# Kernel optimization log

Measured on AMD Instinct MI355X. Metric: run time of the kernel, lower is better.

## Reference

```python
import jax, jax.numpy as jnp
import numpy as np

N, D, ED, E, G, S, H = 16384, 128, 32, 262144, 32, 512, 4
HD = D // H

def _ln(x, g, b, eps=1e-5):
    m = jnp.mean(x, -1, keepdims=True)
    v = jnp.mean((x - m) ** 2, -1, keepdims=True)
    return (x - m) * jax.lax.rsqrt(v + eps) * g + b

def setup_inputs() -> dict:
    key = jax.random.key(0)
    ks = jax.random.split(key, 12)
    r = lambda k, sh: jax.random.normal(k, sh, jnp.float32) * 0.02
    return dict(
        x=jax.random.normal(ks[0], (N, D), jnp.float32),
        edge_index=jax.random.randint(ks[1], (2, E), 0, N),
        edge_attr=jax.random.normal(ks[2], (E, ED), jnp.float32),
        batch=jnp.repeat(jnp.arange(G), S),  # equal-size graphs -> dense batch is a reshape
        gnn_g=jnp.ones((D,), jnp.float32), gnn_b=jnp.zeros((D,), jnp.float32),
        msg_w1=r(ks[3], (2 * D + ED, 2 * D)), msg_b1=jnp.zeros((2 * D,), jnp.float32),
        msg_w2=r(ks[4], (2 * D, D)), msg_b2=jnp.zeros((D,), jnp.float32),
        upd_w1=r(ks[5], (2 * D, D)), upd_b1=jnp.zeros((D,), jnp.float32),
        upd_w2=r(ks[6], (D, D)), upd_b2=jnp.zeros((D,), jnp.float32),
        in_w=r(ks[7], (D, 3 * D)), in_b=jnp.zeros((3 * D,), jnp.float32),
        out_w=r(ks[8], (D, D)), out_b=jnp.zeros((D,), jnp.float32),
        ffn_w1=r(ks[9], (D, 2 * D)), ffn_b1=jnp.zeros((2 * D,), jnp.float32),
        ffn_w2=r(ks[10], (2 * D, D)), ffn_b2=jnp.zeros((D,), jnp.float32),
        n1_g=jnp.ones((D,), jnp.float32), n1_b=jnp.zeros((D,), jnp.float32),
        n2_g=jnp.ones((D,), jnp.float32), n2_b=jnp.zeros((D,), jnp.float32),
    )

def reference(x, edge_index, edge_attr, batch, gnn_g, gnn_b,
              msg_w1, msg_b1, msg_w2, msg_b2, upd_w1, upd_b1, upd_w2, upd_b2,
              in_w, in_b, out_w, out_b, ffn_w1, ffn_b1, ffn_w2, ffn_b2,
              n1_g, n1_b, n2_g, n2_b):
    gelu = lambda t: jax.nn.gelu(t, approximate=False)  # torch nn.GELU default (erf)
    src, dst = edge_index[0], edge_index[1]  # PyG: x_j = source, x_i = target
    # --- local GNN (InteractionLayer), dropout=0 ---
    xn = _ln(x, gnn_g, gnn_b)
    msg_in = jnp.concatenate([xn[dst], xn[src], edge_attr], -1)  # [E, 2D+ED]
    msg = gelu(msg_in @ msg_w1 + msg_b1) @ msg_w2 + msg_b2       # [E, D]
    aggr = jax.ops.segment_sum(msg, dst, num_segments=N)          # scatter-add to targets
    h_local = gelu(jnp.concatenate([xn, aggr], -1) @ upd_w1 + upd_b1) @ upd_w2 + upd_b2
    # --- global self-attention over per-graph dense batch (no padding: equal sizes) ---
    hd = x.reshape(G, S, D)
    qkv = hd @ in_w + in_b
    q, k, v = jnp.split(qkv, 3, -1)
    scale = np.float32(1.0 / np.sqrt(HD))
    q = q.reshape(G, S, H, HD) * scale
    k = k.reshape(G, S, H, HD)
    v = v.reshape(G, S, H, HD)
    att = jax.nn.softmax(jnp.einsum('gqhd,gkhd->ghqk', q, k), -1)
    o = jnp.einsum('ghqk,gkhd->gqhd', att, v).reshape(G, S, D)
    h_attn = (o @ out_w + out_b).reshape(N, D)
    # --- residual + norms + FFN ---
    h = _ln(x + h_local + h_attn, n1_g, n1_b)
    h = _ln(h + (gelu(h @ ffn_w1 + ffn_b1) @ ffn_w2 + ffn_b2), n2_g, n2_b)
    return h
```

## Files before the change

### kernel.cpp

```cpp
#include <hip/hip_runtime.h>
#include <cmath>

#define N_NODES 16384
#define DIM 128
#define EDIM 32
#define NEDGE 262144
#define NG 32
#define SEQ 512
#define NH 4
#define HD 32
#define CH 32

#define EB 32
#define K1 288
#define K1P 296
#define H1 256
#define H1P 264
#define HP 136
#define UP 264

typedef __bf16 bf16x8 __attribute__((ext_vector_type(8)));
typedef float f32x4 __attribute__((ext_vector_type(4)));

__device__ __forceinline__ unsigned short f2bf(float f) {
    union { float f; unsigned int u; } v; v.f = f;
    unsigned int r = (v.u + 0x7FFFu + ((v.u >> 16) & 1u)) >> 16;
    return (unsigned short)r;
}
__device__ __forceinline__ float bf2f(unsigned short u) {
    union { unsigned int u; float f; } v; v.u = ((unsigned int)u) << 16;
    return v.f;
}

__device__ __forceinline__ float geluf(float x) {
    float z = 0.7978845608f * (x + 0.044715f * x * x * x);
    float e = __expf(2.0f * z);
    float t = 1.0f - 2.0f / (e + 1.0f);
    return 0.5f * x * (1.0f + t);
}

__device__ __forceinline__ float waveSum(float v) {
#pragma unroll
    for (int m = 1; m < 64; m <<= 1) v += __shfl_xor(v, m, 64);
    return v;
}

__global__ __launch_bounds__(256) void ln_rows_bf2(const float* __restrict__ x,
                                                   const float* __restrict__ g,
                                                   const float* __restrict__ b,
                                                   unsigned short* __restrict__ xn_bf,
                                                   unsigned short* __restrict__ x_bf) {
    int wave = threadIdx.x >> 6;
    int lane = threadIdx.x & 63;
    int row = blockIdx.x * 4 + wave;
    const float* xr = x + (size_t)row * DIM;
    float v0 = xr[lane], v1 = xr[lane + 64];
    unsigned short* xbf = x_bf + (size_t)row * DIM;
    xbf[lane] = f2bf(v0);
    xbf[lane + 64] = f2bf(v1);
    float mean = waveSum(v0 + v1) * (1.0f / 128.0f);
    float d0 = v0 - mean, d1 = v1 - mean;
    float var = waveSum(d0 * d0 + d1 * d1) * (1.0f / 128.0f);
    float r = rsqrtf(var + 1e-5f);
    unsigned short* obf = xn_bf + (size_t)row * DIM;
    obf[lane] = f2bf(d0 * r * g[lane] + b[lane]);
    obf[lane + 64] = f2bf(d1 * r * g[lane + 64] + b[lane + 64]);
}

__global__ __launch_bounds__(256) void conv_attr(const float* __restrict__ a,
                                                 unsigned short* __restrict__ abf) {
    size_t i = ((size_t)blockIdx.x * 256 + threadIdx.x) * 8;
    float4 x0 = *(const float4*)&a[i];
    float4 x1 = *(const float4*)&a[i + 4];
    unsigned short r[8];
    r[0] = f2bf(x0.x); r[1] = f2bf(x0.y); r[2] = f2bf(x0.z); r[3] = f2bf(x0.w);
    r[4] = f2bf(x1.x); r[5] = f2bf(x1.y); r[6] = f2bf(x1.z); r[7] = f2bf(x1.w);
    *(uint4*)&abf[i] = *(const uint4*)r;
}

__global__ __launch_bounds__(256) void conv_weights(
    const float* __restrict__ s0, const float* __restrict__ s1,
    const float* __restrict__ s2, const float* __restrict__ s3,
    const float* __restrict__ s4, const float* __restrict__ s5,
    const float* __restrict__ s6, const float* __restrict__ s7,
    unsigned short* __restrict__ d0, unsigned short* __restrict__ d1,
    unsigned short* __restrict__ d2, unsigned short* __restrict__ d3,
    unsigned short* __restrict__ d4, unsigned short* __restrict__ d5,
    unsigned short* __restrict__ d6, unsigned short* __restrict__ d7) {
    int i = blockIdx.x * 256 + threadIdx.x;
    if (i < 73728)        { int k = i >> 8, n = i & 255;                 d0[n * 288 + k] = f2bf(s0[i]); }
    else if (i < 106496)  { int j = i - 73728;  int k = j >> 7, n = j & 127; d1[n * 256 + k] = f2bf(s1[j]); }
    else if (i < 139264)  { int j = i - 106496; int k = j >> 7, n = j & 127; d2[n * 256 + k] = f2bf(s2[j]); }
    else if (i < 155648)  { int j = i - 139264; int k = j >> 7, n = j & 127; d3[n * 128 + k] = f2bf(s3[j]); }
    else if (i < 204800)  { int j = i - 155648; int k = j / 384, n = j - k * 384; d4[n * 128 + k] = f2bf(s4[j]); }
    else if (i < 221184)  { int j = i - 204800; int k = j >> 7, n = j & 127; d5[n * 128 + k] = f2bf(s5[j]); }
    else if (i < 253952)  { int j = i - 221184; int k = j >> 8, n = j & 255; d6[n * 128 + k] = f2bf(s6[j]); }
    else if (i < 286720)  { int j = i - 253952; int k = j >> 7, n = j & 127; d7[n * 256 + k] = f2bf(s7[j]); }
}

__global__ __launch_bounds__(256, 4) void edge_mlp_mfma(const unsigned short* __restrict__ xn_bf,
                                                        const int* __restrict__ ei,
                                                        const unsigned short* __restrict__ attr_bf,
                                                        const unsigned short* __restrict__ w1t,
                                                        const float* __restrict__ b1,
                                                        const unsigned short* __restrict__ w2t,
                                                        const float* __restrict__ b2,
                                                        float* __restrict__ aggr) {
    __shared__ __align__(16) unsigned short in_s[EB][K1P];
    __shared__ __align__(16) unsigned short h_s[EB][H1P];
    __shared__ int ds[EB], ss[EB];
    int t = threadIdx.x;
    int eb0 = blockIdx.x * EB;
    if (t < EB) ds[t] = ei[NEDGE + eb0 + t];
    else if (t < 2 * EB) ss[t - EB] = ei[eb0 + t - EB];
    __syncthreads();
    for (int idx = t; idx < EB * 36; idx += 256) {
        int e = idx / 36;
        int seg = idx - e * 36;
        const unsigned short* src;
        if (seg < 16)      src = xn_bf + (size_t)ds[e] * DIM + seg * 8;
        else if (seg < 32) src = xn_bf + (size_t)ss[e] * DIM + (seg - 16) * 8;
        else               src = attr_bf + (size_t)(eb0 + e) * EDIM + (seg - 32) * 8;
        *(uint4*)&in_s[e][seg * 8] = *(const uint4*)src;
    }
    __syncthreads();

    int w = t >> 6;
    int lane = t & 63;
    int l15 = lane & 15;
    int kq = lane >> 4;

    f32x4 acc[2][4] = {};
    for (int kk = 0; kk < 9; ++kk) {
        bf16x8 a[2], bw[4];
#pragma unroll
        for (int mi = 0; mi < 2; ++mi)
            a[mi] = *(const bf16x8*)&in_s[mi * 16 + l15][kk * 32 + kq * 8];
#pragma unroll
        for (int ni = 0; ni < 4; ++ni)
            bw[ni] = *(const bf16x8*)&w1t[(size_t)((w << 6) + ni * 16 + l15) * K1 + kk * 32 + kq * 8];
#pragma unroll
        for (int mi = 0; mi < 2; ++mi)
#pragma unroll
            for (int ni = 0; ni < 4; ++ni)
                acc[mi][ni] = __builtin_amdgcn_mfma_f32_16x16x32_bf16(a[mi], bw[ni], acc[mi][ni], 0, 0, 0);
    }
#pragma unroll
    for (int mi = 0; mi < 2; ++mi)
#pragma unroll
        for (int ni = 0; ni < 4; ++ni) {
            int col = (w << 6) + ni * 16 + l15;
            float bias = b1[col];
#pragma unroll
            for (int j = 0; j < 4; ++j) {
                int row = mi * 16 + kq * 4 + j;
                h_s[row][col] = f2bf(geluf(acc[mi][ni][j] + bias));
            }
        }
    __syncthreads();

    f32x4 acc2[2][2] = {};
    for (int kk = 0; kk < 8; ++kk) {
        bf16x8 a2[2], bw2[2];
#pragma unroll
        for (int mi = 0; mi < 2; ++mi)
            a2[mi] = *(const bf16x8*)&h_s[mi * 16 + l15][kk * 32 + kq * 8];
#pragma unroll
        for (int ni = 0; ni < 2; ++ni)
            bw2[ni] = *(const bf16x8*)&w2t[(size_t)((w << 5) + ni * 16 + l15) * H1 + kk * 32 + kq * 8];
#pragma unroll
        for (int mi = 0; mi < 2; ++mi)
#pragma unroll
            for (int ni = 0; ni < 2; ++ni)
                acc2[mi][ni] = __builtin_amdgcn_mfma_f32_16x16x32_bf16(a2[mi], bw2[ni], acc2[mi][ni], 0, 0, 0);
    }
#pragma unroll
    for (int mi = 0; mi < 2; ++mi)
#pragma unroll
        for (int ni = 0; ni < 2; ++ni) {
            int col = (w << 5) + ni * 16 + l15;
            float bias = b2[col];
#pragma unroll
            for (int j = 0; j < 4; ++j) {
                int row = mi * 16 + kq * 4 + j;
                atomicAdd(&aggr[(size_t)ds[row] * DIM + col], acc2[mi][ni][j] + bias);
            }
        }
}

__global__ __launch_bounds__(256, 2) void update_mfma(const unsigned short* __restrict__ xn_bf,
                                                      const float* __restrict__ aggr,
                                                      const unsigned short* __restrict__ uw1t,
                                                      const float* __restrict__ b1,
                                                      const unsigned short* __restrict__ uw2t,
                                                      const float* __restrict__ b2,
                                                      float* __restrict__ h_local) {
    __shared__ __align__(16) unsigned short cat_s[64][UP];
    __shared__ __align__(16) unsigned short hu_s[64][HP];
    int t = threadIdx.x;
    int n0 = blockIdx.x * 64;
    for (int idx = t; idx < 64 * 32; idx += 256) {
        int e = idx >> 5, seg = idx & 31;
        if (seg < 16) {
            *(uint4*)&cat_s[e][seg * 8] = *(const uint4*)&xn_bf[(size_t)(n0 + e) * DIM + seg * 8];
        } else {
            const float* src = &aggr[(size_t)(n0 + e) * DIM + (seg - 16) * 8];
            float4 a0 = *(const float4*)src, a1 = *(const float4*)(src + 4);
            unsigned short r[8] = {f2bf(a0.x), f2bf(a0.y), f2bf(a0.z), f2bf(a0.w),
                                   f2bf(a1.x), f2bf(a1.y), f2bf(a1.z), f2bf(a1.w)};
            *(uint4*)&cat_s[e][128 + (seg - 16) * 8] = *(const uint4*)r;
        }
    }
    __syncthreads();
    int w = t >> 6, lane = t & 63, l15 = lane & 15, kq = lane >> 4;

    f32x4 acc[4][2] = {};
    for (int kk = 0; kk < 8; ++kk) {
        bf16x8 a[4], bw[2];
#pragma unroll
        for (int mi = 0; mi < 4; ++mi)
            a[mi] = *(const bf16x8*)&cat_s[mi * 16 + l15][kk * 32 + kq * 8];
#pragma unroll
        for (int ni = 0; ni < 2; ++ni)
            bw[ni] = *(const bf16x8*)&uw1t[(size_t)((w << 5) + ni * 16 + l15) * 256 + kk * 32 + kq * 8];
#pragma unroll
        for (int mi = 0; mi < 4; ++mi)
#pragma unroll
            for (int ni = 0; ni < 2; ++ni)
                acc[mi][ni] = __builtin_amdgcn_mfma_f32_16x16x32_bf16(a[mi], bw[ni], acc[mi][ni], 0, 0, 0);
    }
#pragma unroll
    for (int mi = 0; mi < 4; ++mi)
#pragma unroll
        for (int ni = 0; ni < 2; ++ni) {
            int col = (w << 5) + ni * 16 + l15;
            float bias = b1[col];
#pragma unroll
            for (int j = 0; j < 4; ++j) {
                int row = mi * 16 + kq * 4 + j;
                hu_s[row][col] = f2bf(geluf(acc[mi][ni][j] + bias));
            }
        }
    __syncthreads();

    f32x4 acc2[4][2] = {};
    for (int kk = 0; kk < 4; ++kk) {
        bf16x8 a2[4], bw2[2];
#pragma unroll
        for (int mi = 0; mi < 4; ++mi)
            a2[mi] = *(const bf16x8*)&hu_s[mi * 16 + l15][kk * 32 + kq * 8];
#pragma unroll
        for (int ni = 0; ni < 2; ++ni)
            bw2[ni] = *(const bf16x8*)&uw2t[(size_t)((w << 5) + ni * 16 + l15) * 128 + kk * 32 + kq * 8];
#pragma unroll
        for (int mi = 0; mi < 4; ++mi)
#pragma unroll
            for (int ni = 0; ni < 2; ++ni)
                acc2[mi][ni] = __builtin_amdgcn_mfma_f32_16x16x32_bf16(a2[mi], bw2[ni], acc2[mi][ni], 0, 0, 0);
    }
#pragma unroll
    for (int mi = 0; mi < 4; ++mi)
#pragma unroll
        for (int ni = 0; ni < 2; ++ni) {
            int col = (w << 5) + ni * 16 + l15;
            float bias = b2[col];
#pragma unroll
            for (int j = 0; j < 4; ++j) {
                int row = mi * 16 + kq * 4 + j;
                h_local[(size_t)(n0 + row) * DIM + col] = acc2[mi][ni][j] + bias;
            }
        }
}

__global__ __launch_bounds__(256, 2) void qkv_mfma(const unsigned short* __restrict__ x_bf,
                                                   const unsigned short* __restrict__ iwt,
                                                   const float* __restrict__ b,
                                                   unsigned short* __restrict__ qkv_bf) {
    __shared__ __align__(16) unsigned short x_s[64][HP];
    int t = threadIdx.x;
    int n0 = blockIdx.x * 64;
    for (int idx = t; idx < 64 * 16; idx += 256) {
        int e = idx >> 4, seg = idx & 15;
        *(uint4*)&x_s[e][seg * 8] = *(const uint4*)&x_bf[(size_t)(n0 + e) * DIM + seg * 8];
    }
    __syncthreads();
    int w = t >> 6, lane = t & 63, l15 = lane & 15, kq = lane >> 4;

    f32x4 acc[4][6] = {};
    for (int kk = 0; kk < 4; ++kk) {
        bf16x8 a[4], bw[6];
#pragma unroll
        for (int mi = 0; mi < 4; ++mi)
            a[mi] = *(const bf16x8*)&x_s[mi * 16 + l15][kk * 32 + kq * 8];
#pragma unroll
        for (int ni = 0; ni < 6; ++ni)
            bw[ni] = *(const bf16x8*)&iwt[(size_t)(w * 96 + ni * 16 + l15) * 128 + kk * 32 + kq * 8];
#pragma unroll
        for (int mi = 0; mi < 4; ++mi)
#pragma unroll
            for (int ni = 0; ni < 6; ++ni)
                acc[mi][ni] = __builtin_amdgcn_mfma_f32_16x16x32_bf16(a[mi], bw[ni], acc[mi][ni], 0, 0, 0);
    }
#pragma unroll
    for (int mi = 0; mi < 4; ++mi)
#pragma unroll
        for (int ni = 0; ni < 6; ++ni) {
            int col = w * 96 + ni * 16 + l15;
            float bias = b[col];
#pragma unroll
            for (int j = 0; j < 4; ++j) {
                int row = mi * 16 + kq * 4 + j;
                qkv_bf[(size_t)(n0 + row) * 384 + col] = f2bf(acc[mi][ni][j] + bias);
            }
        }
}

__global__ __launch_bounds__(256) void attn_flash(const unsigned short* __restrict__ qkv,
                                                  float* __restrict__ o) {
    int bid = blockIdx.x;
    int quarter = bid & 3;
    int h = (bid >> 2) & 3;
    int g = bid >> 4;
    int t = threadIdx.x;
    int qi = t & 127;
    int sp = t >> 7;
    int sq = quarter * 128 + qi;
    int nq = g * SEQ + sq;

    __shared__ __align__(16) float k_s[2][CH][HD];
    __shared__ __align__(16) float v_s[2][CH][HD];
    __shared__ float merge_s[128][34];

    float qv[HD];
    const unsigned short* qr = qkv + (size_t)nq * 384 + h * HD;
#pragma unroll
    for (int d0 = 0; d0 < HD; d0 += 8) {
        uint4 raw = *(const uint4*)&qr[d0];
        const unsigned short* rs = (const unsigned short*)&raw;
#pragma unroll
        for (int j = 0; j < 8; ++j) qv[d0 + j] = bf2f(rs[j]);
    }
    const float scale = 0.17677669529663687f;
#pragma unroll
    for (int d = 0; d < HD; ++d) qv[d] *= scale;

    float m = -1e30f, l = 0.0f;
    float oacc[HD];
#pragma unroll
    for (int d = 0; d < HD; ++d) oacc[d] = 0.0f;

    int base_j = sp * 256;
    int r = qi >> 3;
    int c4 = (qi & 7) * 4;
    for (int c0 = 0; c0 < 256; c0 += CH) {
        __syncthreads();
#pragma unroll
        for (int p = 0; p < CH; p += 16) {
            int j = base_j + c0 + p + r;
            const unsigned short* kr = qkv + (size_t)(g * SEQ + j) * 384 + 128 + h * HD;
            const unsigned short* vr = qkv + (size_t)(g * SEQ + j) * 384 + 256 + h * HD;
            uint2 kraw = *(const uint2*)&kr[c4];
            uint2 vraw = *(const uint2*)&vr[c4];
            const unsigned short* kp = (const unsigned short*)&kraw;
            const unsigned short* vp = (const unsigned short*)&vraw;
            float4 kf = {bf2f(kp[0]), bf2f(kp[1]), bf2f(kp[2]), bf2f(kp[3])};
            float4 vf = {bf2f(vp[0]), bf2f(vp[1]), bf2f(vp[2]), bf2f(vp[3])};
            *(float4*)&k_s[sp][p + r][c4] = kf;
            *(float4*)&v_s[sp][p + r][c4] = vf;
        }
        __syncthreads();
        float sc[CH];
#pragma unroll
        for (int j = 0; j < CH; ++j) {
            float s = 0.0f;
#pragma unroll
            for (int d = 0; d < HD; ++d) s = fmaf(qv[d], k_s[sp][j][d], s);
            sc[j] = s;
        }
        float cm = sc[0];
#pragma unroll
        for (int j = 1; j < CH; ++j) cm = fmaxf(cm, sc[j]);
        float mn = fmaxf(m, cm);
        float corr = __expf(m - mn);
        l *= corr;
#pragma unroll
        for (int d = 0; d < HD; ++d) oacc[d] *= corr;
#pragma unroll
        for (int j = 0; j < CH; ++j) {
            float p = __expf(sc[j] - mn);
            l += p;
#pragma unroll
            for (int d = 0; d < HD; ++d) oacc[d] = fmaf(p, v_s[sp][j][d], oacc[d]);
        }
        m = mn;
    }
    __syncthreads();
    if (sp == 1) {
        merge_s[qi][0] = m;
        merge_s[qi][1] = l;
#pragma unroll
        for (int d = 0; d < HD; ++d) merge_s[qi][2 + d] = oacc[d];
    }
    __syncthreads();
    if (sp == 0) {
        float m1 = merge_s[qi][0], l1 = merge_s[qi][1];
        float mn = fmaxf(m, m1);
        float cc0 = __expf(m - mn), cc1 = __expf(m1 - mn);
        float inv = 1.0f / (cc0 * l + cc1 * l1);
        float* orow = o + (size_t)nq * DIM + h * HD;
#pragma unroll
        for (int d = 0; d < HD; ++d)
            orow[d] = (cc0 * oacc[d] + cc1 * merge_s[qi][2 + d]) * inv;
    }
}

__global__ __launch_bounds__(256, 2) void proj_res_ln_mfma(const float* __restrict__ x,
                                                           const float* __restrict__ h_local,
                                                           const float* __restrict__ o,
                                                           const unsigned short* __restrict__ owt,
                                                           const float* __restrict__ ob,
                                                           const float* __restrict__ g1,
                                                           const float* __restrict__ bb1,
                                                           float* __restrict__ h1) {
    __shared__ __align__(16) unsigned short o_s[64][HP];
    __shared__ float y_s[64][132];
    int t = threadIdx.x;
    int n0 = blockIdx.x * 64;
    for (int idx = t; idx < 64 * 16; idx += 256) {
        int e = idx >> 4, seg = idx & 15;
        const float* src = &o[(size_t)(n0 + e) * DIM + seg * 8];
        float4 a0 = *(const float4*)src, a1 = *(const float4*)(src + 4);
        unsigned short rr[8] = {f2bf(a0.x), f2bf(a0.y), f2bf(a0.z), f2bf(a0.w),
                                f2bf(a1.x), f2bf(a1.y), f2bf(a1.z), f2bf(a1.w)};
        *(uint4*)&o_s[e][seg * 8] = *(const uint4*)rr;
    }
    __syncthreads();
    int w = t >> 6, lane = t & 63, l15 = lane & 15, kq = lane >> 4;

    f32x4 acc[4][2] = {};
    for (int kk = 0; kk < 4; ++kk) {
        bf16x8 a[4], bw[2];
#pragma unroll
        for (int mi = 0; mi < 4; ++mi)
            a[mi] = *(const bf16x8*)&o_s[mi * 16 + l15][kk * 32 + kq * 8];
#pragma unroll
        for (int ni = 0; ni < 2; ++ni)
            bw[ni] = *(const bf16x8*)&owt[(size_t)((w << 5) + ni * 16 + l15) * 128 + kk * 32 + kq * 8];
#pragma unroll
        for (int mi = 0; mi < 4; ++mi)
#pragma unroll
            for (int ni = 0; ni < 2; ++ni)
                acc[mi][ni] = __builtin_amdgcn_mfma_f32_16x16x32_bf16(a[mi], bw[ni], acc[mi][ni], 0, 0, 0);
    }
#pragma unroll
    for (int mi = 0; mi < 4; ++mi)
#pragma unroll
        for (int ni = 0; ni < 2; ++ni) {
            int col = (w << 5) + ni * 16 + l15;
            float bias = ob[col];
#pragma unroll
            for (int j = 0; j < 4; ++j) {
                int row = mi * 16 + kq * 4 + j;
                size_t gi = (size_t)(n0 + row) * DIM + col;
                y_s[row][col] = x[gi] + h_local[gi] + acc[mi][ni][j] + bias;
            }
        }
    __syncthreads();
    for (int rr = 0; rr < 16; ++rr) {
        int row = (w << 4) + rr;
        float v0 = y_s[row][lane], v1 = y_s[row][lane + 64];
        float mean = waveSum(v0 + v1) * (1.0f / 128.0f);
        float d0 = v0 - mean, d1 = v1 - mean;
        float var = waveSum(d0 * d0 + d1 * d1) * (1.0f / 128.0f);
        float rs = rsqrtf(var + 1e-5f);
        float* hrow = h1 + (size_t)(n0 + row) * DIM;
        hrow[lane] = d0 * rs * g1[lane] + bb1[lane];
        hrow[lane + 64] = d1 * rs * g1[lane + 64] + bb1[lane + 64];
    }
}

__global__ __launch_bounds__(256, 1) void ffn_ln_mfma(const float* __restrict__ h1,
                                                      const unsigned short* __restrict__ fw1t,
                                                      const float* __restrict__ fb1,
                                                      const unsigned short* __restrict__ fw2t,
                                                      const float* __restrict__ fb2,
                                                      const float* __restrict__ g2,
                                                      const float* __restrict__ b2n,
                                                      float* __restrict__ out) {
    __shared__ __align__(16) unsigned short h_s[64][HP];
    __shared__ __align__(16) unsigned short hid_s[64][UP];
    __shared__ float y_s[64][132];
    int t = threadIdx.x;
    int n0 = blockIdx.x * 64;
    for (int idx = t; idx < 64 * 16; idx += 256) {
        int e = idx >> 4, seg = idx & 15;
        const float* src = &h1[(size_t)(n0 + e) * DIM + seg * 8];
        float4 a0 = *(const float4*)src, a1 = *(const float4*)(src + 4);
        unsigned short rr[8] = {f2bf(a0.x), f2bf(a0.y), f2bf(a0.z), f2bf(a0.w),
                                f2bf(a1.x), f2bf(a1.y), f2bf(a1.z), f2bf(a1.w)};
        *(uint4*)&h_s[e][seg * 8] = *(const uint4*)rr;
    }
    __syncthreads();
    int w = t >> 6, lane = t & 63, l15 = lane & 15, kq = lane >> 4;

    f32x4 acc[4][4] = {};
    for (int kk = 0; kk < 4; ++kk) {
        bf16x8 a[4], bw[4];
#pragma unroll
        for (int mi = 0; mi < 4; ++mi)
            a[mi] = *(const bf16x8*)&h_s[mi * 16 + l15][kk * 32 + kq * 8];
#pragma unroll
        for (int ni = 0; ni < 4; ++ni)
            bw[ni] = *(const bf16x8*)&fw1t[(size_t)((w << 6) + ni * 16 + l15) * 128 + kk * 32 + kq * 8];
#pragma unroll
        for (int mi = 0; mi < 4; ++mi)
#pragma unroll
            for (int ni = 0; ni < 4; ++ni)
                acc[mi][ni] = __builtin_amdgcn_mfma_f32_16x16x32_bf16(a[mi], bw[ni], acc[mi][ni], 0, 0, 0);
    }
#pragma unroll
    for (int mi = 0; mi < 4; ++mi)
#pragma unroll
        for (int ni = 0; ni < 4; ++ni) {
            int col = (w << 6) + ni * 16 + l15;
            float bias = fb1[col];
#pragma unroll
            for (int j = 0; j < 4; ++j) {
                int row = mi * 16 + kq * 4 + j;
                hid_s[row][col] = f2bf(geluf(acc[mi][ni][j] + bias));
            }
        }
    __syncthreads();

    f32x4 acc2[4][2] = {};
    for (int kk = 0; kk < 8; ++kk) {
        bf16x8 a2[4], bw2[2];
#pragma unroll
        for (int mi = 0; mi < 4; ++mi)
            a2[mi] = *(const bf16x8*)&hid_s[mi * 16 + l15][kk * 32 + kq * 8];
#pragma unroll
        for (int ni = 0; ni < 2; ++ni)
            bw2[ni] = *(const bf16x8*)&fw2t[(size_t)((w << 5) + ni * 16 + l15) * 256 + kk * 32 + kq * 8];
#pragma unroll
        for (int mi = 0; mi < 4; ++mi)
#pragma unroll
            for (int ni = 0; ni < 2; ++ni)
                acc2[mi][ni] = __builtin_amdgcn_mfma_f32_16x16x32_bf16(a2[mi], bw2[ni], acc2[mi][ni], 0, 0, 0);
    }
#pragma unroll
    for (int mi = 0; mi < 4; ++mi)
#pragma unroll
        for (int ni = 0; ni < 2; ++ni) {
            int col = (w << 5) + ni * 16 + l15;
            float bias = fb2[col];
#pragma unroll
            for (int j = 0; j < 4; ++j) {
                int row = mi * 16 + kq * 4 + j;
                y_s[row][col] = h1[(size_t)(n0 + row) * DIM + col] + acc2[mi][ni][j] + bias;
            }
        }
    __syncthreads();
    for (int rr = 0; rr < 16; ++rr) {
        int row = (w << 4) + rr;
        float v0 = y_s[row][lane], v1 = y_s[row][lane + 64];
        float mean = waveSum(v0 + v1) * (1.0f / 128.0f);
        float d0 = v0 - mean, d1 = v1 - mean;
        float var = waveSum(d0 * d0 + d1 * d1) * (1.0f / 128.0f);
        float rs = rsqrtf(var + 1e-5f);
        float* orow = out + (size_t)(n0 + row) * DIM;
        orow[lane] = d0 * rs * g2[lane] + b2n[lane];
        orow[lane + 64] = d1 * rs * g2[lane + 64] + b2n[lane + 64];
    }
}

extern "C" void kernel_launch(void* const* d_in, const int* in_sizes, int n_in,
                              void* d_out, int out_size, void* d_ws, size_t ws_size,
                              hipStream_t stream) {
    const float* x      = (const float*)d_in[0];
    const int*   ei     = (const int*)d_in[1];
    const float* attr   = (const float*)d_in[2];
    const float* gnn_g  = (const float*)d_in[4];
    const float* gnn_b  = (const float*)d_in[5];
    const float* msg_w1 = (const float*)d_in[6];
    const float* msg_b1 = (const float*)d_in[7];
    const float* msg_w2 = (const float*)d_in[8];
    const float* msg_b2 = (const float*)d_in[9];
    const float* upd_w1 = (const float*)d_in[10];
    const float* upd_b1 = (const float*)d_in[11];
    const float* upd_w2 = (const float*)d_in[12];
    const float* upd_b2 = (const float*)d_in[13];
    const float* in_w   = (const float*)d_in[14];
    const float* in_b   = (const float*)d_in[15];
    const float* out_w  = (const float*)d_in[16];
    const float* out_b  = (const float*)d_in[17];
    const float* ffn_w1 = (const float*)d_in[18];
    const float* ffn_b1 = (const float*)d_in[19];
    const float* ffn_w2 = (const float*)d_in[20];
    const float* ffn_b2 = (const float*)d_in[21];
    const float* n1_g   = (const float*)d_in[22];
    const float* n1_b   = (const float*)d_in[23];
    const float* n2_g   = (const float*)d_in[24];
    const float* n2_b   = (const float*)d_in[25];
    float* out = (float*)d_out;
    float* ws = (float*)d_ws;

    float* aggr    = ws;
    float* h_local = ws + 2097152;
    unsigned short* qkv_bf = (unsigned short*)(ws + 4194304);
    float* o       = ws + 5767168;
    float* h1      = ws + 7864320;
    unsigned short* xn_bf  = (unsigned short*)(ws + 9961472);
    unsigned short* x_bf   = (unsigned short*)(ws + 11010048);
    unsigned short* w1t    = (unsigned short*)(ws + 12058624);
    unsigned short* w2t    = (unsigned short*)(ws + 12095488);
    unsigned short* uw1t   = (unsigned short*)(ws + 12111872);
    unsigned short* uw2t   = (unsigned short*)(ws + 12128256);
    unsigned short* iwt    = (unsigned short*)(ws + 12136448);
    unsigned short* owt    = (unsigned short*)(ws + 12161024);
    unsigned short* fw1t   = (unsigned short*)(ws + 12169216);
    unsigned short* fw2t   = (unsigned short*)(ws + 12185600);
    unsigned short* attr_bf = (unsigned short*)(ws + 12582912);

    hipMemsetAsync(aggr, 0, (size_t)N_NODES * DIM * sizeof(float), stream);
    ln_rows_bf2<<<N_NODES / 4, 256, 0, stream>>>(x, gnn_g, gnn_b, xn_bf, x_bf);
    conv_attr<<<(NEDGE * EDIM) / (256 * 8), 256, 0, stream>>>(attr, attr_bf);
    conv_weights<<<1120, 256, 0, stream>>>(msg_w1, msg_w2, upd_w1, upd_w2, in_w, out_w, ffn_w1, ffn_w2,
                                           w1t, w2t, uw1t, uw2t, iwt, owt, fw1t, fw2t);
    edge_mlp_mfma<<<NEDGE / EB, 256, 0, stream>>>(xn_bf, ei, attr_bf, w1t, msg_b1, w2t, msg_b2, aggr);
    update_mfma<<<N_NODES / 64, 256, 0, stream>>>(xn_bf, aggr, uw1t, upd_b1, uw2t, upd_b2, h_local);
    qkv_mfma<<<N_NODES / 64, 256, 0, stream>>>(x_bf, iwt, in_b, qkv_bf);
    attn_flash<<<NG * NH * 4, 256, 0, stream>>>(qkv_bf, o);
    proj_res_ln_mfma<<<N_NODES / 64, 256, 0, stream>>>(x, h_local, o, owt, out_b, n1_g, n1_b, h1);
    ffn_ln_mfma<<<N_NODES / 64, 256, 0, stream>>>(h1, fw1t, ffn_b1, fw2t, ffn_b2, n2_g, n2_b, out);
}
```

Baseline: 462.6 us.

## Rewrite attention as MFMA flash attention with shared-memory K and transposed V

Replaces the scalar per-thread flash attention with a wave-level MFMA version. Each block stages the whole head's K and a transposed V for its graph in LDS as bf16, computes QK^T and PV with 16x16x32 bf16 MFMAs, and keeps an online softmax using cross-lane shuffles. P is rounded to bf16 through LDS before the PV product. This is meant to cut the FMA-bound scalar dot products and the repeated fp32 K/V staging, at the cost of lower precision in P and more LDS per block.

```diff
diff --git a/kernel.cpp b/kernel.cpp
--- a/kernel.cpp
+++ b/kernel.cpp
@@ -9,7 +9,6 @@
 #define SEQ 512
 #define NH 4
 #define HD 32
-#define CH 32
 
 #define EB 32
 #define K1 288
@@ -315,103 +314,106 @@
         }
 }
 
-__global__ __launch_bounds__(256) void attn_flash(const unsigned short* __restrict__ qkv,
-                                                  float* __restrict__ o) {
+__global__ __launch_bounds__(256, 2) void attn_mfma(const unsigned short* __restrict__ qkv,
+                                                    float* __restrict__ o) {
     int bid = blockIdx.x;
-    int quarter = bid & 3;
+    int qb = bid & 3;
     int h = (bid >> 2) & 3;
     int g = bid >> 4;
     int t = threadIdx.x;
-    int qi = t & 127;
-    int sp = t >> 7;
-    int sq = quarter * 128 + qi;
-    int nq = g * SEQ + sq;
-
-    __shared__ __align__(16) float k_s[2][CH][HD];
-    __shared__ __align__(16) float v_s[2][CH][HD];
-    __shared__ float merge_s[128][34];
-
-    float qv[HD];
-    const unsigned short* qr = qkv + (size_t)nq * 384 + h * HD;
-#pragma unroll
-    for (int d0 = 0; d0 < HD; d0 += 8) {
-        uint4 raw = *(const uint4*)&qr[d0];
-        const unsigned short* rs = (const unsigned short*)&raw;
-#pragma unroll
-        for (int j = 0; j < 8; ++j) qv[d0 + j] = bf2f(rs[j]);
-    }
+    int w = t >> 6, lane = t & 63, l15 = lane & 15, kq = lane >> 4;
+
+    __shared__ __align__(16) unsigned short k_s[SEQ][34];
+    __shared__ __align__(16) unsigned short vT_s[HD][516];
+    __shared__ __align__(16) unsigned short p_s[4][32][36];
+
+    for (int idx = t; idx < SEQ * 4; idx += 256) {
+        int key = idx >> 2, seg = idx & 3;
+        *(uint4*)&k_s[key][seg * 8] =
+            *(const uint4*)&qkv[(size_t)(g * SEQ + key) * 384 + 128 + h * HD + seg * 8];
+    }
+    for (int idx = t; idx < SEQ * 4; idx += 256) {
+        int key = idx >> 2, seg = idx & 3;
+        uint4 raw = *(const uint4*)&qkv[(size_t)(g * SEQ + key) * 384 + 256 + h * HD + seg * 8];
+        const unsigned short* rp = (const unsigned short*)&raw;
+#pragma unroll
+        for (int j = 0; j < 8; ++j) vT_s[seg * 8 + j][key] = rp[j];
+    }
+    int qrow0 = g * SEQ + qb * 128 + w * 32;
+    bf16x8 qA[2];
+#pragma unroll
+    for (int mi = 0; mi < 2; ++mi)
+        qA[mi] = *(const bf16x8*)&qkv[(size_t)(qrow0 + mi * 16 + l15) * 384 + h * HD + kq * 8];
+    __syncthreads();
+
     const float scale = 0.17677669529663687f;
-#pragma unroll
-    for (int d = 0; d < HD; ++d) qv[d] *= scale;
-
-    float m = -1e30f, l = 0.0f;
-    float oacc[HD];
-#pragma unroll
-    for (int d = 0; d < HD; ++d) oacc[d] = 0.0f;
-
-    int base_j = sp * 256;
-    int r = qi >> 3;
-    int c4 = (qi & 7) * 4;
-    for (int c0 = 0; c0 < 256; c0 += CH) {
-        __syncthreads();
-#pragma unroll
-        for (int p = 0; p < CH; p += 16) {
-            int j = base_j + c0 + p + r;
-            const unsigned short* kr = qkv + (size_t)(g * SEQ + j) * 384 + 128 + h * HD;
-            const unsigned short* vr = qkv + (size_t)(g * SEQ + j) * 384 + 256 + h * HD;
-            uint2 kraw = *(const uint2*)&kr[c4];
-            uint2 vraw = *(const uint2*)&vr[c4];
-            const unsigned short* kp = (const unsigned short*)&kraw;
-            const unsigned short* vp = (const unsigned short*)&vraw;
-            float4 kf = {bf2f(kp[0]), bf2f(kp[1]), bf2f(kp[2]), bf2f(kp[3])};
-            float4 vf = {bf2f(vp[0]), bf2f(vp[1]), bf2f(vp[2]), bf2f(vp[3])};
-            *(float4*)&k_s[sp][p + r][c4] = kf;
-            *(float4*)&v_s[sp][p + r][c4] = vf;
-        }
-        __syncthreads();
-        float sc[CH];
-#pragma unroll
-        for (int j = 0; j < CH; ++j) {
-            float s = 0.0f;
-#pragma unroll
-            for (int d = 0; d < HD; ++d) s = fmaf(qv[d], k_s[sp][j][d], s);
-            sc[j] = s;
-        }
-        float cm = sc[0];
-#pragma unroll
-        for (int j = 1; j < CH; ++j) cm = fmaxf(cm, sc[j]);
-        float mn = fmaxf(m, cm);
-        float corr = __expf(m - mn);
-        l *= corr;
-#pragma unroll
-        for (int d = 0; d < HD; ++d) oacc[d] *= corr;
-#pragma unroll
-        for (int j = 0; j < CH; ++j) {
-            float p = __expf(sc[j] - mn);
-            l += p;
-#pragma unroll
-            for (int d = 0; d < HD; ++d) oacc[d] = fmaf(p, v_s[sp][j][d], oacc[d]);
-        }
-        m = mn;
-    }
-    __syncthreads();
-    if (sp == 1) {
-        merge_s[qi][0] = m;
-        merge_s[qi][1] = l;
-#pragma unroll
-        for (int d = 0; d < HD; ++d) merge_s[qi][2 + d] = oacc[d];
-    }
-    __syncthreads();
-    if (sp == 0) {
-        float m1 = merge_s[qi][0], l1 = merge_s[qi][1];
-        float mn = fmaxf(m, m1);
-        float cc0 = __expf(m - mn), cc1 = __expf(m1 - mn);
-        float inv = 1.0f / (cc0 * l + cc1 * l1);
-        float* orow = o + (size_t)nq * DIM + h * HD;
-#pragma unroll
-        for (int d = 0; d < HD; ++d)
-            orow[d] = (cc0 * oacc[d] + cc1 * merge_s[qi][2 + d]) * inv;
-    }
+    float m[2][4], l[2][4];
+    f32x4 oa[2][2] = {};
+#pragma unroll
+    for (int mi = 0; mi < 2; ++mi)
+#pragma unroll
+        for (int j = 0; j < 4; ++j) { m[mi][j] = -1e30f; l[mi][j] = 0.0f; }
+
+    for (int kt = 0; kt < 16; ++kt) {
+        bf16x8 kB[2];
+#pragma unroll
+        for (int ni = 0; ni < 2; ++ni)
+            kB[ni] = *(const bf16x8*)&k_s[kt * 32 + ni * 16 + l15][kq * 8];
+        f32x4 s[2][2] = {};
+#pragma unroll
+        for (int mi = 0; mi < 2; ++mi)
+#pragma unroll
+            for (int ni = 0; ni < 2; ++ni)
+                s[mi][ni] = __builtin_amdgcn_mfma_f32_16x16x32_bf16(qA[mi], kB[ni], s[mi][ni], 0, 0, 0);
+#pragma unroll
+        for (int mi = 0; mi < 2; ++mi) {
+#pragma unroll
+            for (int j = 0; j < 4; ++j) {
+                float s0 = s[mi][0][j] * scale;
+                float s1 = s[mi][1][j] * scale;
+                float cm = fmaxf(s0, s1);
+#pragma unroll
+                for (int msk = 1; msk < 16; msk <<= 1) cm = fmaxf(cm, __shfl_xor(cm, msk, 64));
+                float mn = fmaxf(m[mi][j], cm);
+                float corr = __expf(m[mi][j] - mn);
+                float p0 = __expf(s0 - mn);
+                float p1 = __expf(s1 - mn);
+                float rs = p0 + p1;
+#pragma unroll
+                for (int msk = 1; msk < 16; msk <<= 1) rs += __shfl_xor(rs, msk, 64);
+                l[mi][j] = l[mi][j] * corr + rs;
+                m[mi][j] = mn;
+#pragma unroll
+                for (int nd = 0; nd < 2; ++nd) oa[mi][nd][j] *= corr;
+                int prow = mi * 16 + kq * 4 + j;
+                p_s[w][prow][l15] = f2bf(p0);
+                p_s[w][prow][l15 + 16] = f2bf(p1);
+            }
+        }
+        bf16x8 pA[2], vB[2];
+#pragma unroll
+        for (int mi = 0; mi < 2; ++mi)
+            pA[mi] = *(const bf16x8*)&p_s[w][mi * 16 + l15][kq * 8];
+#pragma unroll
+        for (int nd = 0; nd < 2; ++nd)
+            vB[nd] = *(const bf16x8*)&vT_s[nd * 16 + l15][kt * 32 + kq * 8];
+#pragma unroll
+        for (int mi = 0; mi < 2; ++mi)
+#pragma unroll
+            for (int nd = 0; nd < 2; ++nd)
+                oa[mi][nd] = __builtin_amdgcn_mfma_f32_16x16x32_bf16(pA[mi], vB[nd], oa[mi][nd], 0, 0, 0);
+    }
+#pragma unroll
+    for (int mi = 0; mi < 2; ++mi)
+#pragma unroll
+        for (int j = 0; j < 4; ++j) {
+            float inv = 1.0f / l[mi][j];
+            int row = qrow0 + mi * 16 + kq * 4 + j;
+            float* orow = o + (size_t)row * DIM + h * HD;
+#pragma unroll
+            for (int nd = 0; nd < 2; ++nd)
+                orow[nd * 16 + l15] = oa[mi][nd][j] * inv;
+        }
 }
 
 __global__ __launch_bounds__(256, 2) void proj_res_ln_mfma(const float* __restrict__ x,
@@ -629,7 +631,7 @@
     edge_mlp_mfma<<<NEDGE / EB, 256, 0, stream>>>(xn_bf, ei, attr_bf, w1t, msg_b1, w2t, msg_b2, aggr);
     update_mfma<<<N_NODES / 64, 256, 0, stream>>>(xn_bf, aggr, uw1t, upd_b1, uw2t, upd_b2, h_local);
     qkv_mfma<<<N_NODES / 64, 256, 0, stream>>>(x_bf, iwt, in_b, qkv_bf);
-    attn_flash<<<NG * NH * 4, 256, 0, stream>>>(qkv_bf, o);
+    attn_mfma<<<NG * NH * 4, 256, 0, stream>>>(qkv_bf, o);
     proj_res_ln_mfma<<<N_NODES / 64, 256, 0, stream>>>(x, h_local, o, owt, out_b, n1_g, n1_b, h1);
     ffn_ln_mfma<<<N_NODES / 64, 256, 0, stream>>>(h1, fw1t, ffn_b1, fw2t, ffn_b2, n2_g, n2_b, out);
 }
```

Result: faster. 418.6 us (-9.5%).
